# Performance work log

Hardware: AMD Instinct MI355X
Metric: run time of the kernel (lower is better)

Reference implementation:

```python
import jax, jax.numpy as jnp
import numpy as np
from jax import lax

K = 3
K2 = 9
PAD = 1
GN_GROUPS = 32
GN_EPS = 1e-5
COS_EPS = 1e-8


def conv2d(x, w):
    # 3x3, stride 1, pad 1, NCHW/OIHW
    return lax.conv_general_dilated(x, w, (1, 1), ((PAD, PAD), (PAD, PAD)),
                                    dimension_numbers=('NCHW', 'OIHW', 'NCHW'))


def group_norm(x, gamma, beta):
    N, C, H, W = x.shape
    xg = x.reshape(N, GN_GROUPS, C // GN_GROUPS, H, W)
    m = xg.mean(axis=(2, 3, 4), keepdims=True)
    v = xg.var(axis=(2, 3, 4), keepdims=True)
    xn = ((xg - m) * lax.rsqrt(v + GN_EPS)).reshape(N, C, H, W)
    return xn * gamma[None, :, None, None] + beta[None, :, None, None]


def deform_conv(x, offset, weight):
    # mmcv DeformConv, deformable_groups=1: offset [N, 2*K2, H, W] as (dy,dx) per kernel tap.
    N, C, H, W = x.shape
    off = offset.reshape(N, K2, 2, H, W)
    dy, dx = off[:, :, 0], off[:, :, 1]              # [N,K2,H,W]
    ky, kx = jnp.meshgrid(jnp.arange(K), jnp.arange(K), indexing='ij')
    ky = ky.reshape(K2).astype(x.dtype)
    kx = kx.reshape(K2).astype(x.dtype)
    hh = jnp.arange(H, dtype=x.dtype)
    ww = jnp.arange(W, dtype=x.dtype)
    # absolute (fractional) sample positions per output pixel and kernel tap
    py = hh[None, None, :, None] - PAD + ky[None, :, None, None] + dy   # [N,K2,H,W]
    px = ww[None, None, None, :] - PAD + kx[None, :, None, None] + dx
    y0 = jnp.floor(py)
    x0 = jnp.floor(px)
    ay = py - y0
    ax = px - x0
    xf = x.reshape(N, C, H * W)
    sampled = jnp.zeros((N, C, K2, H, W), x.dtype)
    for oy, wy in ((y0, 1.0 - ay), (y0 + 1.0, ay)):
        for ox, wx in ((x0, 1.0 - ax), (x0 + 1.0, ax)):
            valid = (oy >= 0) & (oy <= H - 1) & (ox >= 0) & (ox <= W - 1)
            yi = jnp.clip(oy, 0, H - 1).astype(jnp.int32)
            xi = jnp.clip(ox, 0, W - 1).astype(jnp.int32)
            idx = (yi * W + xi).reshape(N, 1, K2 * H * W)
            v = jnp.take_along_axis(xf, idx, axis=2).reshape(N, C, K2, H, W)
            w = jnp.where(valid, wy * wx, 0.0)[:, None]   # zero padding outside
            sampled = sampled + v * w
    O = weight.shape[0]
    return jnp.einsum('nckhw,ock->nohw', sampled, weight.reshape(O, C, K2))


def cos_sim(a, b):
    num = jnp.sum(a * b, axis=1)
    na = jnp.sqrt(jnp.sum(a * a, axis=1))
    nb = jnp.sqrt(jnp.sum(b * b, axis=1))
    return num / jnp.maximum(na * nb, COS_EPS)   # [N,H,W]


def agg(support, reference, layers):
    f = jnp.concatenate([support, reference], axis=1)
    for ow, ob, dw, gg, gb in layers[:3]:
        off = conv2d(f, ow) + ob[None, :, None, None]
        f = jax.nn.relu(group_norm(deform_conv(f, off, dw), gg, gb))
    ow, ob, dw, gg, gb = layers[3]
    off = conv2d(f, ow) + ob[None, :, None, None]
    return jax.nn.relu(group_norm(deform_conv(support, off, dw), gg, gb))


def setup_inputs() -> dict:
    key = jax.random.key(0)
    ks = jax.random.split(key, 16)
    C_in, C_out, H, W = 512, 256, 96, 96
    rn = lambda k, shape, s: jax.random.normal(k, shape, jnp.float32) * s
    inp = {'datas': jax.random.normal(ks[0], (2, C_out, H, W), jnp.float32)}
    i = 1
    for n in (1, 2, 3):
        inp[f'off{n}_w'] = rn(ks[i], (18, C_in, 3, 3), 0.01); i += 1
        inp[f'off{n}_b'] = jnp.zeros((18,), jnp.float32)
        inp[f'dcn{n}_w'] = rn(ks[i], (C_in, C_in, 3, 3), 0.02); i += 1
        inp[f'gn{n}_g'] = jnp.ones((C_in,), jnp.float32)
        inp[f'gn{n}_b'] = jnp.zeros((C_in,), jnp.float32)
    inp['off4_w'] = rn(ks[i], (18, C_in, 3, 3), 0.01); i += 1
    inp['off4_b'] = jnp.zeros((18,), jnp.float32)
    inp['dcn4_w'] = rn(ks[i], (C_out, C_out, 3, 3), 0.02); i += 1
    inp['gn4_g'] = jnp.ones((C_out,), jnp.float32)
    inp['gn4_b'] = jnp.zeros((C_out,), jnp.float32)
    return inp


def reference(datas, off1_w, off1_b, dcn1_w, gn1_g, gn1_b,
              off2_w, off2_b, dcn2_w, gn2_g, gn2_b,
              off3_w, off3_b, dcn3_w, gn3_g, gn3_b,
              off4_w, off4_b, dcn4_w, gn4_g, gn4_b):
    layers = [(off1_w, off1_b, dcn1_w, gn1_g, gn1_b),
              (off2_w, off2_b, dcn2_w, gn2_g, gn2_b),
              (off3_w, off3_b, dcn3_w, gn3_g, gn3_b),
              (off4_w, off4_b, dcn4_w, gn4_g, gn4_b)]
    support = datas[:1]
    reference_f = datas[1:]
    tt = agg(reference_f, reference_f, layers)   # [1,C_out,H,W]
    ttw = cos_sim(tt, tt)[:, None]               # [1,1,H,W]
    tk = agg(support, reference_f, layers)
    tkw = cos_sim(tt, tk)[:, None]
    w = jax.nn.softmax(jnp.stack([ttw, tkw], axis=0), axis=0)  # [2,1,1,H,W]
    f = jnp.stack([tt, tk], axis=0)                            # [2,1,C,H,W]
    return jnp.sum(w * f, axis=0)
```

## Files before the change

kernel.cpp:

```cpp
#include <hip/hip_runtime.h>
#include <math.h>

#define HW 9216
#define WIDTH 96
#define FSTRIDE (512*HW)
#define RSTRIDE (256*HW)
#define TABSTRIDE (9*HW)
#define PXP 12544
#define FTPROWS 12800

typedef __attribute__((ext_vector_type(8))) short bf16x8;
typedef __attribute__((ext_vector_type(4))) float f32x4;
typedef __attribute__((ext_vector_type(8))) unsigned short u16x8;

__device__ __forceinline__ unsigned short f2bf(float f) {
  unsigned int u = __float_as_uint(f);
  u += 0x7FFFu + ((u >> 16) & 1u);
  return (unsigned short)(u >> 16);
}
__device__ __forceinline__ float bf2f(unsigned short s) {
  return __uint_as_float(((unsigned int)s) << 16);
}

#define GLDS(g, l) __builtin_amdgcn_global_load_lds( \
    (const __attribute__((address_space(1))) unsigned int*)(g), \
    (__attribute__((address_space(3))) unsigned int*)(l), 16, 0, 0)

__global__ void k_zero(unsigned short* p, unsigned int n8) {
  unsigned int i = blockIdx.x * 256 + threadIdx.x;
  if (i < n8) ((u16x8*)p)[i] = (u16x8){0, 0, 0, 0, 0, 0, 0, 0};
}

__global__ void __launch_bounds__(256) k_mkftp_cat(
    const float* __restrict__ lo0, const float* __restrict__ lo1,
    const float* __restrict__ hi, unsigned short* __restrict__ dst,
    int C, int CB) {
  const int b = blockIdx.z;
  const float* lo = b ? lo1 : lo0;
  unsigned short* d = dst + (size_t)b * FTPROWS * C + 128 * C;
  const int px0 = blockIdx.x * 64, c0 = blockIdx.y * 64;
  __shared__ float tile[64][65];
  const int t = threadIdx.x;
#pragma unroll
  for (int rep = 0; rep < 16; ++rep) {
    int idx = rep * 256 + t;
    int cl = idx >> 6, pl = idx & 63;
    int cg = c0 + cl;
    const float* s = (cg < CB) ? (lo + (size_t)cg * HW) : (hi + (size_t)(cg - CB) * HW);
    tile[cl][pl] = s[px0 + pl];
  }
  __syncthreads();
  const int pl = t >> 2, cu = (t & 3) * 16;
  const int px = px0 + pl;
  const int h = px / WIDTH, w = px - h * WIDTH;
  const size_t pxp = (size_t)(h + 1) * 128 + (w + 1);
  u16x8 o0, o1;
#pragma unroll
  for (int j = 0; j < 8; ++j) o0[j] = f2bf(tile[cu + j][pl]);
#pragma unroll
  for (int j = 0; j < 8; ++j) o1[j] = f2bf(tile[cu + 8 + j][pl]);
  unsigned short* p = d + pxp * C + c0 + cu;
  *(u16x8*)p = o0;
  *(u16x8*)(p + 8) = o1;
}

__global__ void __launch_bounds__(256) k_mkftp_gn(
    const float* __restrict__ y, const float2* __restrict__ stat,
    const float* __restrict__ gamma, const float* __restrict__ beta,
    unsigned short* __restrict__ dst) {
  const int C = 512;
  const int b = blockIdx.z;
  unsigned short* d = dst + (size_t)b * FTPROWS * C + 128 * C;
  const int px0 = blockIdx.x * 64, c0 = blockIdx.y * 64;
  __shared__ float tile[64][65];
  const int t = threadIdx.x;
#pragma unroll
  for (int rep = 0; rep < 16; ++rep) {
    int idx = rep * 256 + t;
    int cl = idx >> 6, pl = idx & 63;
    int cg = c0 + cl;
    float2 st = stat[b * 32 + (cg >> 4)];
    float v = y[(size_t)b * FSTRIDE + (size_t)cg * HW + px0 + pl];
    v = (v - st.x) * st.y * gamma[cg] + beta[cg];
    tile[cl][pl] = fmaxf(v, 0.f);
  }
  __syncthreads();
  const int pl = t >> 2, cu = (t & 3) * 16;
  const int px = px0 + pl;
  const int h = px / WIDTH, w = px - h * WIDTH;
  const size_t pxp = (size_t)(h + 1) * 128 + (w + 1);
  u16x8 o0, o1;
#pragma unroll
  for (int j = 0; j < 8; ++j) o0[j] = f2bf(tile[cu + j][pl]);
#pragma unroll
  for (int j = 0; j < 8; ++j) o1[j] = f2bf(tile[cu + 8 + j][pl]);
  unsigned short* p = d + pxp * C + c0 + cu;
  *(u16x8*)p = o0;
  *(u16x8*)(p + 8) = o1;
}

__global__ void k_prepW(const float* __restrict__ ow, unsigned short* __restrict__ Wt) {
  int i = blockIdx.x * 256 + threadIdx.x;
  int k = i / (32 * 512), r = i - k * 32 * 512;
  int oc = r / 512, c = r - oc * 512;
  Wt[i] = (oc < 18) ? f2bf(ow[((size_t)oc * 512 + c) * 9 + k]) : (unsigned short)0;
}

__global__ void __launch_bounds__(256) k_offmm(const unsigned short* __restrict__ ftp,
                                               const unsigned short* __restrict__ Wt,
                                               float* __restrict__ part) {
  const int C = 512;
  __shared__ unsigned short As[128 * 64];
  __shared__ unsigned short Bs[32 * 64];
  const int tid = threadIdx.x;
  const int lane = tid & 63, wv = tid >> 6;
  const int b = blockIdx.z, ks = blockIdx.y;
  const int pxp0 = 128 + blockIdx.x * 128;
  const unsigned short* fb = ftp + (size_t)b * FTPROWS * C + 128 * C;

  const int lr = lane >> 3;
  const int lu = lane & 7;
  const int fr = lane & 15, hi = lane >> 4;

  f32x4 acc[2][2];
#pragma unroll
  for (int i = 0; i < 2; ++i)
#pragma unroll
    for (int j = 0; j < 2; ++j) acc[i][j] = (f32x4){0.f, 0.f, 0.f, 0.f};

  for (int kt = 0; kt < 3; ++kt) {
    const int k = ks * 3 + kt;
    const int dlt = (k / 3 - 1) * 128 + (k % 3 - 1);
    for (int c0 = 0; c0 < C; c0 += 64) {
#pragma unroll
      for (int q = 0; q < 4; ++q) {
        int row = wv * 32 + q * 8 + lr;
        int su = lu ^ (row & 7);
        GLDS(fb + (size_t)(pxp0 + dlt + row) * C + c0 + su * 8,
             (char*)As + (wv * 32 + q * 8) * 128);
      }
      {
        int row = wv * 8 + lr;
        int su = lu ^ (row & 7);
        GLDS(Wt + ((size_t)k * 32 + row) * C + c0 + su * 8,
             (char*)Bs + wv * 8 * 128);
      }
      asm volatile("s_waitcnt vmcnt(0)" ::: "memory");
      __syncthreads();
#pragma unroll
      for (int kk = 0; kk < 2; ++kk) {
        bf16x8 a[2], bb[2];
#pragma unroll
        for (int i = 0; i < 2; ++i) {
          int row = wv * 32 + i * 16 + fr;
          a[i] = *(const bf16x8*)&As[row * 64 + (((kk * 4 + hi) ^ (row & 7)) * 8)];
        }
#pragma unroll
        for (int j = 0; j < 2; ++j) {
          int row = j * 16 + fr;
          bb[j] = *(const bf16x8*)&Bs[row * 64 + (((kk * 4 + hi) ^ (row & 7)) * 8)];
        }
#pragma unroll
        for (int i = 0; i < 2; ++i)
#pragma unroll
          for (int j = 0; j < 2; ++j)
            acc[i][j] = __builtin_amdgcn_mfma_f32_16x16x32_bf16(a[i], bb[j], acc[i][j], 0, 0, 0);
      }
      __syncthreads();
    }
  }

  float* pb = part + ((size_t)(b * 3 + ks)) * PXP * 32;
#pragma unroll
  for (int i = 0; i < 2; ++i)
#pragma unroll
    for (int j = 0; j < 2; ++j) {
      int row0 = pxp0 + wv * 32 + i * 16 + hi * 4;
      int col = j * 16 + fr;
#pragma unroll
      for (int q = 0; q < 4; ++q)
        pb[(size_t)(row0 + q) * 32 + col] = acc[i][j][q];
    }
}

__global__ void k_table(const float* __restrict__ part, const float* __restrict__ ob,
                        int4* __restrict__ tabi, float4* __restrict__ tabw) {
  int b = blockIdx.z, k = blockIdx.y;
  int px = blockIdx.x * 256 + threadIdx.x;
  int h = px / WIDTH, w = px - h * WIDTH;
  size_t pxp = (size_t)(h + 1) * 128 + (w + 1);
  const float* pb = part + (size_t)b * 3 * PXP * 32 + pxp * 32;
  float dy = ob[2 * k] + pb[2 * k] + pb[(size_t)PXP * 32 + 2 * k] + pb[2 * (size_t)PXP * 32 + 2 * k];
  float dx = ob[2 * k + 1] + pb[2 * k + 1] + pb[(size_t)PXP * 32 + 2 * k + 1] + pb[2 * (size_t)PXP * 32 + 2 * k + 1];
  float py = (float)(h - 1 + k / 3) + dy;
  float pxx = (float)(w - 1 + k % 3) + dx;
  float y0 = floorf(py), x0 = floorf(pxx);
  float ay = py - y0, ax = pxx - x0;
  float wy[2] = {1.f - ay, ay}, wx[2] = {1.f - ax, ax};
  int idx[4]; float wt[4];
#pragma unroll
  for (int t = 0; t < 4; ++t) {
    float oy = y0 + (float)(t >> 1);
    float ox = x0 + (float)(t & 1);
    bool valid = (oy >= 0.f) && (oy <= 95.f) && (ox >= 0.f) && (ox <= 95.f);
    int yi = (int)fminf(fmaxf(oy, 0.f), 95.f);
    int xi = (int)fminf(fmaxf(ox, 0.f), 95.f);
    idx[t] = (yi + 1) * 128 + (xi + 1);
    wt[t] = valid ? wy[t >> 1] * wx[t & 1] : 0.f;
  }
  size_t e = (size_t)b * TABSTRIDE + (size_t)k * HW + px;
  tabi[e] = make_int4(idx[0], idx[1], idx[2], idx[3]);
  tabw[e] = make_float4(wt[0], wt[1], wt[2], wt[3]);
}

__global__ void __launch_bounds__(256) k_sample_t(
    const unsigned short* __restrict__ ftp,
    const int4* __restrict__ tabi, const float4* __restrict__ tabw,
    unsigned short* __restrict__ samp, int C, int kbase, int rowK) {
  const int z = blockIdx.z;
  const int b = z & 1, kloc = z >> 1;
  const int k = kbase + kloc;
  const int t = threadIdx.x;
  const int px = blockIdx.x * 64 + (t >> 2);
  const int c = blockIdx.y * 64 + (t & 3) * 16;
  const unsigned short* fb = ftp + (size_t)b * FTPROWS * C + 128 * C;
  size_t e = (size_t)b * TABSTRIDE + (size_t)k * HW + px;
  int4 id = tabi[e];
  float4 wt = tabw[e];
  float acc[16];
#pragma unroll
  for (int j = 0; j < 16; ++j) acc[j] = 0.f;
  const int ids[4] = {id.x, id.y, id.z, id.w};
  const float wts[4] = {wt.x, wt.y, wt.z, wt.w};
#pragma unroll
  for (int s = 0; s < 4; ++s) {
    const unsigned short* p = fb + (size_t)ids[s] * C + c;
    u16x8 v0 = *(const u16x8*)p;
    u16x8 v1 = *(const u16x8*)(p + 8);
    float wgt = wts[s];
#pragma unroll
    for (int j = 0; j < 8; ++j) acc[j] += wgt * bf2f(v0[j]);
#pragma unroll
    for (int j = 0; j < 8; ++j) acc[8 + j] += wgt * bf2f(v1[j]);
  }
  u16x8 o0, o1;
#pragma unroll
  for (int j = 0; j < 8; ++j) o0[j] = f2bf(acc[j]);
#pragma unroll
  for (int j = 0; j < 8; ++j) o1[j] = f2bf(acc[8 + j]);
  unsigned short* dst = samp + ((size_t)b * HW + px) * rowK + kloc * C + c;
  *(u16x8*)dst = o0;
  *(u16x8*)(dst + 8) = o1;
}

__global__ void k_prepA(const float* __restrict__ dw, unsigned short* __restrict__ Ap,
                        int C) {
  int o = blockIdx.x * 256 + threadIdx.x;
  int K = 9 * C;
  int m = o / K, r = o - m * K;
  int k = r / C, c = r - k * C;
  Ap[o] = f2bf(dw[((size_t)m * C + c) * 9 + k]);
}

__device__ __forceinline__ void stage_ab96(const unsigned short* __restrict__ Ag,
                                           const unsigned short* __restrict__ Bg,
                                           int lda, int rowK, int kt,
                                           unsigned short* as_, unsigned short* bs_,
                                           int wv, int lane) {
  const int lr = lane >> 2;
  const int lu = lane & 3;
#pragma unroll
  for (int q = 0; q < 2; ++q) {
    int row = wv * 32 + q * 16 + lr;
    int su = lu ^ ((row >> 1) & 3);
    GLDS(Ag + (size_t)row * lda + kt + su * 8, (char*)as_ + (wv * 2 + q) * 1024);
  }
  const int nb = (wv < 2) ? 2 : 1;
  const int bu0 = (wv < 2) ? (2 * wv) : (wv + 2);
  for (int q = 0; q < nb; ++q) {
    int unit = bu0 + q;
    int row = unit * 16 + lr;
    int su = lu ^ ((row >> 1) & 3);
    GLDS(Bg + (size_t)row * rowK + kt + su * 8, (char*)bs_ + unit * 1024);
  }
}

__global__ void __launch_bounds__(256) k_dcgemm(
    const unsigned short* __restrict__ Ap, const unsigned short* __restrict__ Bt,
    float* __restrict__ Y, int lda, int rowK, int aOff, int accum) {
  __shared__ unsigned short As[3][128 * 32];
  __shared__ unsigned short Bs[3][96 * 32];
  const int tid = threadIdx.x;
  const int lane = tid & 63, wv = tid >> 6;

  const int nwg = gridDim.x;
  const int cpx = nwg >> 3;
  const int bid = blockIdx.x;
  const int l = (bid & 7) * cpx + (bid >> 3);
  const int nm = nwg / 192;
  const int m_i = l % nm;
  const int rest = l / nm;
  const int n_i = rest % 96;
  const int b = rest / 96;

  const int m0 = m_i << 7, n0 = n_i * 96;
  const unsigned short* Ag = Ap + (size_t)m0 * lda + aOff;
  const unsigned short* Bg = Bt + ((size_t)b * HW + n0) * rowK;

  const int wm = (wv >> 1) * 64, wn = (wv & 1) * 48;
  const int fr = lane & 15, hi = lane >> 4;
  const int nt = rowK >> 5;

  f32x4 acc[4][3];
#pragma unroll
  for (int i = 0; i < 4; ++i)
#pragma unroll
    for (int j = 0; j < 3; ++j) acc[i][j] = (f32x4){0.f, 0.f, 0.f, 0.f};

  stage_ab96(Ag, Bg, lda, rowK, 0,  &As[0][0], &Bs[0][0], wv, lane);
  stage_ab96(Ag, Bg, lda, rowK, 32, &As[1][0], &Bs[1][0], wv, lane);

  for (int t = 0; t < nt; ++t) {
    const int cur = t % 3;
    if (t + 2 < nt) {
      stage_ab96(Ag, Bg, lda, rowK, (t + 2) << 5, &As[(t + 2) % 3][0],
                 &Bs[(t + 2) % 3][0], wv, lane);
      if (wv < 2) asm volatile("s_waitcnt vmcnt(8)" ::: "memory");
      else        asm volatile("s_waitcnt vmcnt(6)" ::: "memory");
    } else if (t + 1 < nt) {
      if (wv < 2) asm volatile("s_waitcnt vmcnt(4)" ::: "memory");
      else        asm volatile("s_waitcnt vmcnt(3)" ::: "memory");
    } else {
      asm volatile("s_waitcnt vmcnt(0)" ::: "memory");
    }
    __builtin_amdgcn_s_barrier();
    __builtin_amdgcn_sched_barrier(0);
    bf16x8 a[4], bb[3];
#pragma unroll
    for (int i = 0; i < 4; ++i) {
      int row = wm + i * 16 + fr;
      a[i] = *(const bf16x8*)&As[cur][row * 32 + ((hi ^ ((row >> 1) & 3)) * 8)];
    }
#pragma unroll
    for (int j = 0; j < 3; ++j) {
      int row = wn + j * 16 + fr;
      bb[j] = *(const bf16x8*)&Bs[cur][row * 32 + ((hi ^ ((row >> 1) & 3)) * 8)];
    }
    __builtin_amdgcn_s_setprio(1);
#pragma unroll
    for (int i = 0; i < 4; ++i)
#pragma unroll
      for (int j = 0; j < 3; ++j)
        acc[i][j] = __builtin_amdgcn_mfma_f32_16x16x32_bf16(a[i], bb[j], acc[i][j], 0, 0, 0);
    __builtin_amdgcn_s_setprio(0);
    __builtin_amdgcn_s_barrier();
  }

  float* Yb = Y + (size_t)b * FSTRIDE;
  const int orow = m0 + wm + hi * 4;
  const int ocol = n0 + wn + fr;
#pragma unroll
  for (int i = 0; i < 4; ++i) {
#pragma unroll
    for (int j = 0; j < 3; ++j) {
      float* p = Yb + (size_t)(orow + i * 16) * HW + ocol + j * 16;
#pragma unroll
      for (int q = 0; q < 4; ++q) {
        float v = acc[i][j][q];
        if (accum) v += p[(size_t)q * HW];
        p[(size_t)q * HW] = v;
      }
    }
  }
}

__global__ void __launch_bounds__(256) k_gnstats1(const float* __restrict__ y,
                                                  float2* __restrict__ part, int CperG) {
  const int b = blockIdx.z, g = blockIdx.x, ch = blockIdx.y;
  const int n = CperG * HW;
  const int cs = n >> 4;
  const int cs4 = cs >> 2;
  const float4* p = (const float4*)(y + (size_t)b * FSTRIDE + (size_t)g * n + (size_t)ch * cs);
  float s = 0.f, q = 0.f;
  for (int i = threadIdx.x; i < cs4; i += 256) {
    float4 v = p[i];
    s += v.x + v.y + v.z + v.w;
    q += v.x * v.x + v.y * v.y + v.z * v.z + v.w * v.w;
  }
  __shared__ float ss[256], qs[256];
  ss[threadIdx.x] = s; qs[threadIdx.x] = q;
  __syncthreads();
  for (int d = 128; d > 0; d >>= 1) {
    if (threadIdx.x < d) { ss[threadIdx.x] += ss[threadIdx.x + d]; qs[threadIdx.x] += qs[threadIdx.x + d]; }
    __syncthreads();
  }
  if (threadIdx.x == 0) part[((b << 5) + g) * 16 + ch] = make_float2(ss[0], qs[0]);
}

__global__ void k_gnfin(const float2* __restrict__ part, float2* __restrict__ stat,
                        int CperG) {
  int t = threadIdx.x;
  float s = 0.f, q = 0.f;
#pragma unroll
  for (int j = 0; j < 16; ++j) { float2 v = part[t * 16 + j]; s += v.x; q += v.y; }
  float n = (float)(CperG * HW);
  float m = s / n;
  float var = q / n - m * m;
  stat[t] = make_float2(m, rsqrtf(var + 1e-5f));
}

__global__ void k_gnapply(const float* __restrict__ y, const float2* __restrict__ stat,
                          const float* __restrict__ gamma, const float* __restrict__ beta,
                          float* __restrict__ out, int CperG, size_t ostride) {
  int b = blockIdx.z;
  int i = (blockIdx.x * 256 + threadIdx.x) * 4;
  int c = i / HW;
  float2 st = stat[b * 32 + c / CperG];
  float ga = gamma[c], be = beta[c];
  float4 v = *(const float4*)(y + (size_t)b * FSTRIDE + i);
  v.x = fmaxf((v.x - st.x) * st.y * ga + be, 0.f);
  v.y = fmaxf((v.y - st.x) * st.y * ga + be, 0.f);
  v.z = fmaxf((v.z - st.x) * st.y * ga + be, 0.f);
  v.w = fmaxf((v.w - st.x) * st.y * ga + be, 0.f);
  *(float4*)(out + (size_t)b * ostride + i) = v;
}

__global__ void k_cos1(const float* __restrict__ res, float4* __restrict__ part) {
  int px = blockIdx.x * 256 + threadIdx.x;
  int cc = blockIdx.y;
  float saa = 0.f, sbb = 0.f, sab = 0.f;
  for (int c = cc * 32; c < cc * 32 + 32; ++c) {
    float a = res[(size_t)c * HW + px];
    float bb = res[2 * (size_t)RSTRIDE + (size_t)c * HW + px];
    saa += a * a; sbb += bb * bb; sab += a * bb;
  }
  part[(size_t)cc * HW + px] = make_float4(saa, sbb, sab, 0.f);
}

__global__ void k_cos2(const float4* __restrict__ part, float* __restrict__ wpix) {
  int px = blockIdx.x * 256 + threadIdx.x;
  float saa = 0.f, sbb = 0.f, sab = 0.f;
#pragma unroll
  for (int cc = 0; cc < 8; ++cc) {
    float4 v = part[(size_t)cc * HW + px];
    saa += v.x; sbb += v.y; sab += v.z;
  }
  float na = sqrtf(saa), nb = sqrtf(sbb);
  float ttw = saa / fmaxf(na * na, 1e-8f);
  float tkw = sab / fmaxf(na * nb, 1e-8f);
  float m = fmaxf(ttw, tkw);
  float e0 = expf(ttw - m), e1 = expf(tkw - m);
  wpix[px] = e0 / (e0 + e1);
}

__global__ void k_combine(const float* __restrict__ res, const float* __restrict__ wpix,
                          float* __restrict__ out) {
  int i = blockIdx.x * 256 + threadIdx.x;
  int px = i % HW;
  float w0 = wpix[px];
  out[i] = w0 * res[i] + (1.f - w0) * res[2 * (size_t)RSTRIDE + i];
}

extern "C" void kernel_launch(void* const* d_in, const int* in_sizes, int n_in,
                              void* d_out, int out_size, void* d_ws, size_t ws_size,
                              hipStream_t stream) {
  const float* datas = (const float*)d_in[0];
  const float* ow[4] = {(const float*)d_in[1], (const float*)d_in[6],
                        (const float*)d_in[11], (const float*)d_in[16]};
  const float* ob[4] = {(const float*)d_in[2], (const float*)d_in[7],
                        (const float*)d_in[12], (const float*)d_in[17]};
  const float* dw[4] = {(const float*)d_in[3], (const float*)d_in[8],
                        (const float*)d_in[13], (const float*)d_in[18]};
  const float* gg[4] = {(const float*)d_in[4], (const float*)d_in[9],
                        (const float*)d_in[14], (const float*)d_in[19]};
  const float* gb[4] = {(const float*)d_in[5], (const float*)d_in[10],
                        (const float*)d_in[15], (const float*)d_in[20]};

  const int fullk = (ws_size >= 255100000ull) ? 1 : 0;
  const size_t sampN = fullk ? (2 * (size_t)HW * 4608) : (2 * (size_t)HW * 1536);

  float* ws = (float*)d_ws;
  float* y     = ws;
  float* offp3 = y + 2 * (size_t)FSTRIDE;
  float4* tabw = (float4*)(offp3 + 2 * 3 * (size_t)PXP * 32);
  int4*   tabi = (int4*)(tabw + 2 * (size_t)TABSTRIDE);
  float* wpix = (float*)(tabi + 2 * (size_t)TABSTRIDE);
  float2* stat = (float2*)(wpix + HW);
  float2* gnpart = stat + 64;
  float4* cospart = (float4*)(gnpart + 1024);
  float* endp = (float*)(cospart + 8 * (size_t)HW);
  size_t ofs = ((size_t)(endp - ws) + 3) & ~(size_t)3;
  unsigned short* samp = (unsigned short*)(ws + ofs);
  unsigned short* Ap = samp + sampN;
  unsigned short* Wt = Ap + (size_t)512 * 4608;
  unsigned short* ftp512 = Wt + (size_t)9 * 32 * 512;
  unsigned short* ftp256 = fullk ? (samp + 2 * (size_t)HW * 2304)
                                 : (ftp512 + 2 * (size_t)FTPROWS * 512);

  dim3 blk(256);
  k_zero<<<dim3(2 * FTPROWS * 512 / 8 / 256), blk, 0, stream>>>(ftp512, 2u * FTPROWS * 512 / 8);

  for (int l = 0; l < 4; ++l) {
    const int Cx = (l < 3) ? 512 : 256;
    const int M  = Cx;
    if (l == 0) {
      k_mkftp_cat<<<dim3(144, 8, 2), blk, 0, stream>>>(datas + RSTRIDE, datas,
                                                       datas + RSTRIDE, ftp512, 512, 256);
    } else {
      k_gnstats1<<<dim3(32, 16, 2), blk, 0, stream>>>(y, gnpart, 16);
      k_gnfin<<<dim3(1), dim3(64), 0, stream>>>(gnpart, stat, 16);
      k_mkftp_gn<<<dim3(144, 8, 2), blk, 0, stream>>>(y, stat, gg[l - 1], gb[l - 1], ftp512);
    }
    k_prepA<<<dim3(M * 9 * Cx / 256), blk, 0, stream>>>(dw[l], Ap, Cx);
    k_prepW<<<dim3(9 * 32 * 512 / 256), blk, 0, stream>>>(ow[l], Wt);
    k_offmm<<<dim3(96, 3, 2), blk, 0, stream>>>(ftp512, Wt, offp3);
    k_table<<<dim3(36, 9, 2), blk, 0, stream>>>(offp3, ob[l], tabi, tabw);
    const unsigned short* sftp;
    if (l < 3) {
      sftp = ftp512;
    } else {
      k_zero<<<dim3(2 * FTPROWS * 256 / 8 / 256), blk, 0, stream>>>(ftp256, 2u * FTPROWS * 256 / 8);
      k_mkftp_cat<<<dim3(144, 4, 2), blk, 0, stream>>>(datas + RSTRIDE, datas,
                                                       datas, ftp256, 256, 256);
      sftp = ftp256;
    }
    const int nch = fullk ? 1 : 3;
    const int nk = 9 / nch;
    const int rowK = nk * Cx;
    for (int ch = 0; ch < nch; ++ch) {
      k_sample_t<<<dim3(144, Cx / 64, 2 * nk), blk, 0, stream>>>(sftp, tabi, tabw, samp,
                                                                 Cx, ch * nk, rowK);
      k_dcgemm<<<dim3((M / 128) * 96 * 2), blk, 0, stream>>>(Ap, samp, y, 9 * Cx, rowK,
                                                             ch * rowK, ch > 0);
    }
  }

  k_gnstats1<<<dim3(32, 16, 2), blk, 0, stream>>>(y, gnpart, 8);
  k_gnfin<<<dim3(1), dim3(64), 0, stream>>>(gnpart, stat, 8);
  float* res = y + RSTRIDE;
  k_gnapply<<<dim3(RSTRIDE / 1024, 1, 2), blk, 0, stream>>>(y, stat, gg[3], gb[3], res,
                                                            8, 2 * (size_t)RSTRIDE);
  k_cos1<<<dim3(36, 8), blk, 0, stream>>>(res, cospart);
  k_cos2<<<dim3(36), blk, 0, stream>>>(cospart, wpix);
  k_combine<<<dim3(RSTRIDE / 256), blk, 0, stream>>>(res, wpix, (float*)d_out);
}
```

Baseline: 996.6 us.

## Store conv outputs in bf16, fuse GroupNorm stats into GEMM epilogue, double-buffer offset GEMM

```diff
diff --git a/kernel.cpp b/kernel.cpp
--- a/kernel.cpp
+++ b/kernel.cpp
@@ -65,7 +65,7 @@
 }
 
 __global__ void __launch_bounds__(256) k_mkftp_gn(
-    const float* __restrict__ y, const float2* __restrict__ stat,
+    const unsigned short* __restrict__ yh, const float2* __restrict__ stat,
     const float* __restrict__ gamma, const float* __restrict__ beta,
     unsigned short* __restrict__ dst) {
   const int C = 512;
@@ -80,7 +80,7 @@
     int cl = idx >> 6, pl = idx & 63;
     int cg = c0 + cl;
     float2 st = stat[b * 32 + (cg >> 4)];
-    float v = y[(size_t)b * FSTRIDE + (size_t)cg * HW + px0 + pl];
+    float v = bf2f(yh[(size_t)b * FSTRIDE + (size_t)cg * HW + px0 + pl]);
     v = (v - st.x) * st.y * gamma[cg] + beta[cg];
     tile[cl][pl] = fmaxf(v, 0.f);
   }
@@ -110,8 +110,8 @@
                                                const unsigned short* __restrict__ Wt,
                                                float* __restrict__ part) {
   const int C = 512;
-  __shared__ unsigned short As[128 * 64];
-  __shared__ unsigned short Bs[32 * 64];
+  __shared__ unsigned short As[2][128 * 64];
+  __shared__ unsigned short Bs[2][32 * 64];
   const int tid = threadIdx.x;
   const int lane = tid & 63, wv = tid >> 6;
   const int b = blockIdx.z, ks = blockIdx.y;
@@ -128,46 +128,56 @@
 #pragma unroll
     for (int j = 0; j < 2; ++j) acc[i][j] = (f32x4){0.f, 0.f, 0.f, 0.f};
 
-  for (int kt = 0; kt < 3; ++kt) {
-    const int k = ks * 3 + kt;
-    const int dlt = (k / 3 - 1) * 128 + (k % 3 - 1);
-    for (int c0 = 0; c0 < C; c0 += 64) {
-#pragma unroll
-      for (int q = 0; q < 4; ++q) {
-        int row = wv * 32 + q * 8 + lr;
-        int su = lu ^ (row & 7);
-        GLDS(fb + (size_t)(pxp0 + dlt + row) * C + c0 + su * 8,
-             (char*)As + (wv * 32 + q * 8) * 128);
+#define OFFMM_STAGE(S, BUF)                                                   \
+  {                                                                           \
+    const int k_ = ks * 3 + ((S) >> 3);                                       \
+    const int dlt_ = (k_ / 3 - 1) * 128 + (k_ % 3 - 1);                       \
+    const int c0_ = ((S) & 7) * 64;                                           \
+    _Pragma("unroll")                                                         \
+    for (int q = 0; q < 4; ++q) {                                             \
+      int row = wv * 32 + q * 8 + lr;                                         \
+      int su = lu ^ (row & 7);                                                \
+      GLDS(fb + (size_t)(pxp0 + dlt_ + row) * C + c0_ + su * 8,               \
+           (char*)&As[BUF][0] + (wv * 32 + q * 8) * 128);                     \
+    }                                                                         \
+    {                                                                         \
+      int row = wv * 8 + lr;                                                  \
+      int su = lu ^ (row & 7);                                                \
+      GLDS(Wt + ((size_t)k_ * 32 + row) * C + c0_ + su * 8,                   \
+           (char*)&Bs[BUF][0] + wv * 8 * 128);                                \
+    }                                                                         \
+  }
+
+  OFFMM_STAGE(0, 0);
+  for (int s = 0; s < 24; ++s) {
+    const int cur = s & 1;
+    if (s + 1 < 24) {
+      OFFMM_STAGE(s + 1, cur ^ 1);
+      asm volatile("s_waitcnt vmcnt(5)" ::: "memory");
+    } else {
+      asm volatile("s_waitcnt vmcnt(0)" ::: "memory");
+    }
+    __builtin_amdgcn_s_barrier();
+#pragma unroll
+    for (int kk = 0; kk < 2; ++kk) {
+      bf16x8 a[2], bb[2];
+#pragma unroll
+      for (int i = 0; i < 2; ++i) {
+        int row = wv * 32 + i * 16 + fr;
+        a[i] = *(const bf16x8*)&As[cur][row * 64 + (((kk * 4 + hi) ^ (row & 7)) * 8)];
       }
-      {
-        int row = wv * 8 + lr;
-        int su = lu ^ (row & 7);
-        GLDS(Wt + ((size_t)k * 32 + row) * C + c0 + su * 8,
-             (char*)Bs + wv * 8 * 128);
+#pragma unroll
+      for (int j = 0; j < 2; ++j) {
+        int row = j * 16 + fr;
+        bb[j] = *(const bf16x8*)&Bs[cur][row * 64 + (((kk * 4 + hi) ^ (row & 7)) * 8)];
       }
-      asm volatile("s_waitcnt vmcnt(0)" ::: "memory");
-      __syncthreads();
-#pragma unroll
-      for (int kk = 0; kk < 2; ++kk) {
-        bf16x8 a[2], bb[2];
-#pragma unroll
-        for (int i = 0; i < 2; ++i) {
-          int row = wv * 32 + i * 16 + fr;
-          a[i] = *(const bf16x8*)&As[row * 64 + (((kk * 4 + hi) ^ (row & 7)) * 8)];
-        }
-#pragma unroll
-        for (int j = 0; j < 2; ++j) {
-          int row = j * 16 + fr;
-          bb[j] = *(const bf16x8*)&Bs[row * 64 + (((kk * 4 + hi) ^ (row & 7)) * 8)];
-        }
-#pragma unroll
-        for (int i = 0; i < 2; ++i)
-#pragma unroll
-          for (int j = 0; j < 2; ++j)
-            acc[i][j] = __builtin_amdgcn_mfma_f32_16x16x32_bf16(a[i], bb[j], acc[i][j], 0, 0, 0);
-      }
-      __syncthreads();
-    }
+#pragma unroll
+      for (int i = 0; i < 2; ++i)
+#pragma unroll
+        for (int j = 0; j < 2; ++j)
+          acc[i][j] = __builtin_amdgcn_mfma_f32_16x16x32_bf16(a[i], bb[j], acc[i][j], 0, 0, 0);
+    }
+    __builtin_amdgcn_s_barrier();
   }
 
   float* pb = part + ((size_t)(b * 3 + ks)) * PXP * 32;
@@ -287,7 +297,8 @@
 
 __global__ void __launch_bounds__(256) k_dcgemm(
     const unsigned short* __restrict__ Ap, const unsigned short* __restrict__ Bt,
-    float* __restrict__ Y, int lda, int rowK, int aOff, int accum) {
+    unsigned short* __restrict__ Yh, float2* __restrict__ gnp,
+    int lda, int rowK, int aOff, int accum, int CperG, int dogn) {
   __shared__ unsigned short As[3][128 * 32];
   __shared__ unsigned short Bs[3][96 * 32];
   const int tid = threadIdx.x;
@@ -356,36 +367,71 @@
     __builtin_amdgcn_s_barrier();
   }
 
-  float* Yb = Y + (size_t)b * FSTRIDE;
+  unsigned short* Yb = Yh + (size_t)b * FSTRIDE;
   const int orow = m0 + wm + hi * 4;
   const int ocol = n0 + wn + fr;
+  float s_[4], q_[4];
+#pragma unroll
+  for (int i = 0; i < 4; ++i) { s_[i] = 0.f; q_[i] = 0.f; }
 #pragma unroll
   for (int i = 0; i < 4; ++i) {
 #pragma unroll
     for (int j = 0; j < 3; ++j) {
-      float* p = Yb + (size_t)(orow + i * 16) * HW + ocol + j * 16;
+      unsigned short* p = Yb + (size_t)(orow + i * 16) * HW + ocol + j * 16;
 #pragma unroll
       for (int q = 0; q < 4; ++q) {
         float v = acc[i][j][q];
-        if (accum) v += p[(size_t)q * HW];
-        p[(size_t)q * HW] = v;
+        if (accum) v += bf2f(p[(size_t)q * HW]);
+        p[(size_t)q * HW] = f2bf(v);
+        s_[i] += v;
+        q_[i] += v * v;
       }
     }
   }
-}
-
-__global__ void __launch_bounds__(256) k_gnstats1(const float* __restrict__ y,
-                                                  float2* __restrict__ part, int CperG) {
+
+  if (dogn) {
+    const int redmax = (CperG == 16) ? 32 : 16;
+#pragma unroll
+    for (int i = 0; i < 4; ++i) {
+      float s = s_[i], q = q_[i];
+      for (int off = 1; off <= redmax; off <<= 1) {
+        s += __shfl_xor(s, off);
+        q += __shfl_xor(q, off);
+      }
+      int row0 = m0 + wm + i * 16 + ((CperG == 8) ? (lane >> 5) * 8 : 0);
+      int g = row0 / CperG;
+      bool writer = (CperG == 16) ? (lane == 0) : ((lane & 31) == 0);
+      if (writer)
+        gnp[(((size_t)(b * 32 + g)) * 96 + n_i) * 2 + (wv & 1)] = make_float2(s, q);
+    }
+  }
+}
+
+__global__ void k_gnfin2(const float2* __restrict__ gnp, float2* __restrict__ stat,
+                         int CperG) {
+  int t = threadIdx.x;
+  float s = 0.f, q = 0.f;
+  for (int j = 0; j < 192; ++j) {
+    float2 v = gnp[(size_t)t * 192 + j];
+    s += v.x; q += v.y;
+  }
+  float n = (float)(CperG * HW);
+  float m = s / n;
+  float var = q / n - m * m;
+  stat[t] = make_float2(m, rsqrtf(var + 1e-5f));
+}
+
+__global__ void __launch_bounds__(256) k_gnstats1h(const unsigned short* __restrict__ yh,
+                                                   float2* __restrict__ part, int CperG) {
   const int b = blockIdx.z, g = blockIdx.x, ch = blockIdx.y;
   const int n = CperG * HW;
-  const int cs = n >> 4;
-  const int cs4 = cs >> 2;
-  const float4* p = (const float4*)(y + (size_t)b * FSTRIDE + (size_t)g * n + (size_t)ch * cs);
+  const int cs8 = (n >> 4) >> 3;
+  const u16x8* p = (const u16x8*)(yh + (size_t)b * FSTRIDE + (size_t)g * n + (size_t)ch * (n >> 4));
   float s = 0.f, q = 0.f;
-  for (int i = threadIdx.x; i < cs4; i += 256) {
-    float4 v = p[i];
-    s += v.x + v.y + v.z + v.w;
-    q += v.x * v.x + v.y * v.y + v.z * v.z + v.w * v.w;
+  for (int i = threadIdx.x; i < cs8; i += 256) {
+    u16x8 v = p[i];
+#pragma unroll
+    for (int j = 0; j < 8; ++j) { float f = bf2f(v[j]); s += f; q += f * f; }
   }
   __shared__ float ss[256], qs[256];
   ss[threadIdx.x] = s; qs[threadIdx.x] = q;
@@ -409,7 +455,8 @@
   stat[t] = make_float2(m, rsqrtf(var + 1e-5f));
 }
 
-__global__ void k_gnapply(const float* __restrict__ y, const float2* __restrict__ stat,
+__global__ void k_gnapply(const unsigned short* __restrict__ yh,
+                          const float2* __restrict__ stat,
                           const float* __restrict__ gamma, const float* __restrict__ beta,
                           float* __restrict__ out, int CperG, size_t ostride) {
   int b = blockIdx.z;
@@ -417,7 +464,8 @@
   int c = i / HW;
   float2 st = stat[b * 32 + c / CperG];
   float ga = gamma[c], be = beta[c];
-  float4 v = *(const float4*)(y + (size_t)b * FSTRIDE + i);
+  ushort4 vv = *(const ushort4*)(yh + (size_t)b * FSTRIDE + i);
+  float4 v = make_float4(bf2f(vv.x), bf2f(vv.y), bf2f(vv.z), bf2f(vv.w));
   v.x = fmaxf((v.x - st.x) * st.y * ga + be, 0.f);
   v.y = fmaxf((v.y - st.x) * st.y * ga + be, 0.f);
   v.z = fmaxf((v.z - st.x) * st.y * ga + be, 0.f);
@@ -431,7 +479,7 @@
   float saa = 0.f, sbb = 0.f, sab = 0.f;
   for (int c = cc * 32; c < cc * 32 + 32; ++c) {
     float a = res[(size_t)c * HW + px];
-    float bb = res[2 * (size_t)RSTRIDE + (size_t)c * HW + px];
+    float bb = res[(size_t)RSTRIDE + (size_t)c * HW + px];
     saa += a * a; sbb += bb * bb; sab += a * bb;
   }
   part[(size_t)cc * HW + px] = make_float4(saa, sbb, sab, 0.f);
@@ -458,7 +506,7 @@
   int i = blockIdx.x * 256 + threadIdx.x;
   int px = i % HW;
   float w0 = wpix[px];
-  out[i] = w0 * res[i] + (1.f - w0) * res[2 * (size_t)RSTRIDE + i];
+  out[i] = w0 * res[i] + (1.f - w0) * res[(size_t)RSTRIDE + i];
 }
 
 extern "C" void kernel_launch(void* const* d_in, const int* in_sizes, int n_in,
@@ -476,17 +524,18 @@
   const float* gb[4] = {(const float*)d_in[5], (const float*)d_in[10],
                         (const float*)d_in[15], (const float*)d_in[20]};
 
-  const int fullk = (ws_size >= 255100000ull) ? 1 : 0;
+  const int fullk = (ws_size >= 236400000ull) ? 1 : 0;
   const size_t sampN = fullk ? (2 * (size_t)HW * 4608) : (2 * (size_t)HW * 1536);
 
   float* ws = (float*)d_ws;
-  float* y     = ws;
-  float* offp3 = y + 2 * (size_t)FSTRIDE;
+  unsigned short* yh = (unsigned short*)ws;
+  float* offp3 = ws + (2 * (size_t)FSTRIDE * 2) / 4;
   float4* tabw = (float4*)(offp3 + 2 * 3 * (size_t)PXP * 32);
   int4*   tabi = (int4*)(tabw + 2 * (size_t)TABSTRIDE);
   float* wpix = (float*)(tabi + 2 * (size_t)TABSTRIDE);
   float2* stat = (float2*)(wpix + HW);
-  float2* gnpart = stat + 64;
+  float2* gnp  = stat + 64;
+  float2* gnpart = gnp + 2 * 32 * 96 * 2;
   float4* cospart = (float4*)(gnpart + 1024);
   float* endp = (float*)(cospart + 8 * (size_t)HW);
   size_t ofs = ((size_t)(endp - ws) + 3) & ~(size_t)3;
@@ -496,27 +545,28 @@
   unsigned short* ftp512 = Wt + (size_t)9 * 32 * 512;
   unsigned short* ftp256 = fullk ? (samp + 2 * (size_t)HW * 2304)
                                  : (ftp512 + 2 * (size_t)FTPROWS * 512);
+  float* res = (float*)(ftp256 + 2 * (size_t)FTPROWS * 256);
 
   dim3 blk(256);
   k_zero<<<dim3(2 * FTPROWS * 512 / 8 / 256), blk, 0, stream>>>(ftp512, 2u * FTPROWS * 512 / 8);
 
-  for (int l = 0; l < 4; ++l) {
-    const int Cx = (l < 3) ? 512 : 256;
+  for (int lyr = 0; lyr < 4; ++lyr) {
+    const int Cx = (lyr < 3) ? 512 : 256;
     const int M  = Cx;
-    if (l == 0) {
+    const int CperG = (lyr < 3) ? 16 : 8;
+    if (lyr == 0) {
       k_mkftp_cat<<<dim3(144, 8, 2), blk, 0, stream>>>(datas + RSTRIDE, datas,
                                                        datas + RSTRIDE, ftp512, 512, 256);
     } else {
-      k_gnstats1<<<dim3(32, 16, 2), blk, 0, stream>>>(y, gnpart, 16);
-      k_gnfin<<<dim3(1), dim3(64), 0, stream>>>(gnpart, stat, 16);
-      k_mkftp_gn<<<dim3(144, 8, 2), blk, 0, stream>>>(y, stat, gg[l - 1], gb[l - 1], ftp512);
-    }
-    k_prepA<<<dim3(M * 9 * Cx / 256), blk, 0, stream>>>(dw[l], Ap, Cx);
-    k_prepW<<<dim3(9 * 32 * 512 / 256), blk, 0, stream>>>(ow[l], Wt);
+      k_mkftp_gn<<<dim3(144, 8, 2), blk, 0, stream>>>(yh, stat, gg[lyr - 1], gb[lyr - 1],
+                                                      ftp512);
+    }
+    k_prepA<<<dim3(M * 9 * Cx / 256), blk, 0, stream>>>(dw[lyr], Ap, Cx);
+    k_prepW<<<dim3(9 * 32 * 512 / 256), blk, 0, stream>>>(ow[lyr], Wt);
     k_offmm<<<dim3(96, 3, 2), blk, 0, stream>>>(ftp512, Wt, offp3);
-    k_table<<<dim3(36, 9, 2), blk, 0, stream>>>(offp3, ob[l], tabi, tabw);
+    k_table<<<dim3(36, 9, 2), blk, 0, stream>>>(offp3, ob[lyr], tabi, tabw);
     const unsigned short* sftp;
-    if (l < 3) {
+    if (lyr < 3) {
       sftp = ftp512;
     } else {
       k_zero<<<dim3(2 * FTPROWS * 256 / 8 / 256), blk, 0, stream>>>(ftp256, 2u * FTPROWS * 256 / 8);
@@ -530,16 +580,20 @@
     for (int ch = 0; ch < nch; ++ch) {
       k_sample_t<<<dim3(144, Cx / 64, 2 * nk), blk, 0, stream>>>(sftp, tabi, tabw, samp,
                                                                  Cx, ch * nk, rowK);
-      k_dcgemm<<<dim3((M / 128) * 96 * 2), blk, 0, stream>>>(Ap, samp, y, 9 * Cx, rowK,
-                                                             ch * rowK, ch > 0);
-    }
-  }
-
-  k_gnstats1<<<dim3(32, 16, 2), blk, 0, stream>>>(y, gnpart, 8);
-  k_gnfin<<<dim3(1), dim3(64), 0, stream>>>(gnpart, stat, 8);
-  float* res = y + RSTRIDE;
-  k_gnapply<<<dim3(RSTRIDE / 1024, 1, 2), blk, 0, stream>>>(y, stat, gg[3], gb[3], res,
-                                                            8, 2 * (size_t)RSTRIDE);
+      k_dcgemm<<<dim3((M / 128) * 96 * 2), blk, 0, stream>>>(
+          Ap, samp, yh, gnp, 9 * Cx, rowK, ch * rowK, ch > 0, CperG,
+          fullk && (ch == nch - 1));
+    }
+    if (fullk) {
+      k_gnfin2<<<dim3(1), dim3(64), 0, stream>>>(gnp, stat, CperG);
+    } else {
+      k_gnstats1h<<<dim3(32, 16, 2), blk, 0, stream>>>(yh, gnpart, CperG);
+      k_gnfin<<<dim3(1), dim3(64), 0, stream>>>(gnpart, stat, CperG);
+    }
+  }
+
+  k_gnapply<<<dim3(RSTRIDE / 1024, 1, 2), blk, 0, stream>>>(yh, stat, gg[3], gb[3], res,
+                                                            8, (size_t)RSTRIDE);
   k_cos1<<<dim3(36, 8), blk, 0, stream>>>(res, cospart);
   k_cos2<<<dim3(36), blk, 0, stream>>>(cospart, wpix);
   k_combine<<<dim3(RSTRIDE / 256), blk, 0, stream>>>(res, wpix, (float*)d_out);
```

Result: no change. 978.4 us (-1.8%).
